# Kernel tuning notes

Hardware: AMD Instinct MI355X
Metric: run time of the kernel (lower is better)

Reference implementation:

```python
import jax, jax.numpy as jnp
import numpy as np

BN_EPS = 1e-5


def setup_inputs() -> dict:
    key = jax.random.key(0)
    k1, k2, k3, k4 = jax.random.split(key, 4)
    N, E, D_IN, D_OUT = 100000, 1600000, 128, 128
    x = jax.random.normal(k1, (N, D_IN), dtype=jnp.float32)
    edge_index = jax.random.randint(k2, (2, E), 0, N, dtype=jnp.int64)
    # GCNConv linear (glorot) + bias (zeros init in PyG)
    W = jax.random.normal(k3, (D_OUT, D_IN), dtype=jnp.float32) * (1.0 / np.sqrt(D_IN))
    b = jnp.zeros((D_OUT,), dtype=jnp.float32)
    # BatchNorm affine params
    gamma = jnp.ones((D_OUT,), dtype=jnp.float32)
    beta = jnp.zeros((D_OUT,), dtype=jnp.float32)
    return {"x": x, "edge_index": edge_index, "W": W, "b": b,
            "gamma": gamma, "beta": beta}


def reference(x, edge_index, W, b, gamma, beta):
    N = x.shape[0]
    # --- GCNConv: add self-loops, symmetric normalization ---
    loop = jnp.arange(N, dtype=edge_index.dtype)
    src = jnp.concatenate([edge_index[0], loop])  # [E+N]
    dst = jnp.concatenate([edge_index[1], loop])  # [E+N]
    deg = jax.ops.segment_sum(jnp.ones_like(dst, dtype=x.dtype), dst,
                              num_segments=N)  # in-degree incl. self-loop
    dinv = jnp.where(deg > 0, jax.lax.rsqrt(deg), 0.0)
    norm = dinv[src] * dinv[dst]  # [E+N]
    # linear transform before propagation (PyG GCNConv)
    h = x @ W.T  # [N, D_OUT]
    agg = jax.ops.segment_sum(h[src] * norm[:, None], dst, num_segments=N)
    out = agg + b
    # --- BatchNorm1d (training mode: batch statistics over nodes) ---
    mean = jnp.mean(out, axis=0)
    var = jnp.var(out, axis=0)
    out = (out - mean) * jax.lax.rsqrt(var + BN_EPS) * gamma + beta
    # --- ReLU, residual, dropout(p=0 -> identity) ---
    out = jax.nn.relu(out)
    out = out + x  # residual (in_dim == out_dim)
    return out
```

## Files before the change

kernel.cpp:

```cpp
#include <hip/hip_runtime.h>
#include <hip/hip_fp16.h>

#define BN_EPS 1e-5f

typedef unsigned int uint32;
typedef __attribute__((ext_vector_type(8))) _Float16 f16x8;
typedef __attribute__((ext_vector_type(4))) float f32x4;

union H2U { __half2 h; uint32 u; };

__device__ __forceinline__ __half2 u2h(uint32 u) { H2U c; c.u = u; return c.h; }
__device__ __forceinline__ uint32 h2u(__half2 h) { H2U c; c.h = h; return c.u; }
__device__ __forceinline__ uint32 pack2h(float a, float b) {
    return h2u(__halves2half2(__float2half_rn(a), __float2half_rn(b)));
}
__device__ __forceinline__ float h2lo(uint32 u) {
    return __half2float(__ushort_as_half((unsigned short)(u & 0xffffu)));
}
__device__ __forceinline__ float h2hi(uint32 u) {
    return __half2float(__ushort_as_half((unsigned short)(u >> 16)));
}


__global__ void __launch_bounds__(256) k_prep(const float4* __restrict__ x4, int nx4,
                                              const float4* __restrict__ w4, int nw4,
                                              const int* __restrict__ dst, int E, int NB,
                                              uint2* __restrict__ xh4, uint2* __restrict__ wh4,
                                              int* __restrict__ bcnt) {
    __shared__ int h[1024];
    int t = threadIdx.x;
    if (blockIdx.x < 256) {
        for (int i = t; i < NB; i += 256) h[i] = 0;
        __syncthreads();
        int c0 = (int)((long long)blockIdx.x * E / 256);
        int c1 = (int)((long long)(blockIdx.x + 1) * E / 256);
        for (int e = c0 + t; e < c1; e += 256) atomicAdd(&h[dst[e] >> 8], 1);
        __syncthreads();
        for (int i = t; i < NB; i += 256)
            if (h[i]) atomicAdd(&bcnt[i], h[i]);
    }
    int idx = blockIdx.x * 256 + t;
    int stride = gridDim.x * 256;
    for (int i = idx; i < nx4; i += stride) {
        float4 v = x4[i];
        xh4[i] = make_uint2(pack2h(v.x, v.y), pack2h(v.z, v.w));
    }
    for (int i = idx; i < nw4; i += stride) {
        float4 v = w4[i];
        wh4[i] = make_uint2(pack2h(v.x, v.y), pack2h(v.z, v.w));
    }
}


__global__ void k_scan1024(const int* __restrict__ in, int n, int* __restrict__ outExcl) {
    __shared__ int s[1024];
    int t = threadIdx.x;
    int v = (t < n) ? in[t] : 0;
    s[t] = v;
    __syncthreads();
    for (int off = 1; off < 1024; off <<= 1) {
        int add = (t >= off) ? s[t - off] : 0;
        __syncthreads();
        s[t] += add;
        __syncthreads();
    }
    if (t < n) outExcl[t] = s[t] - v;
    if (t == n - 1) outExcl[n] = s[t];
}


__global__ void __launch_bounds__(256) k_bscatter(const int* __restrict__ ei, int E, int NB,
                                                  const int* __restrict__ bbase,
                                                  int* __restrict__ bfill,
                                                  uint32* __restrict__ bpack) {
    __shared__ int h[1024];
    int t = threadIdx.x;
    int c0 = (int)((long long)blockIdx.x * E / gridDim.x);
    int c1 = (int)((long long)(blockIdx.x + 1) * E / gridDim.x);
    for (int i = t; i < NB; i += 256) h[i] = 0;
    __syncthreads();
    for (int e = c0 + t; e < c1; e += 256)
        atomicAdd(&h[ei[E + e] >> 8], 1);
    __syncthreads();
    for (int i = t; i < NB; i += 256) {
        int c = h[i];
        if (c > 0) h[i] = bbase[i] + atomicAdd(&bfill[i], c);
    }
    __syncthreads();
    for (int e = c0 + t; e < c1; e += 256) {
        int s = ei[e];
        int d = ei[E + e];
        int b = d >> 8;
        int pos = atomicAdd(&h[b], 1);
        bpack[pos] = ((uint32)(d & 255) << 24) | (uint32)s;
    }
}


__global__ void __launch_bounds__(256) k_csr(const uint32* __restrict__ bpack,
                                             const int* __restrict__ bbase,
                                             int N, int E,
                                             int* __restrict__ rowptr,
                                             uint32* __restrict__ dpk,
                                             int* __restrict__ col) {
    __shared__ int h[256], s[256], cur[256];
    int b = blockIdx.x;
    int t = threadIdx.x;
    int e0 = bbase[b], e1 = bbase[b + 1];
    h[t] = 0;
    __syncthreads();
    for (int e = e0 + t; e < e1; e += 256)
        atomicAdd(&h[bpack[e] >> 24], 1);
    __syncthreads();
    int cnt = h[t];
    s[t] = cnt;
    __syncthreads();
    for (int off = 1; off < 256; off <<= 1) {
        int add = (t >= off) ? s[t - off] : 0;
        __syncthreads();
        s[t] += add;
        __syncthreads();
    }
    int excl = s[t] - cnt;
    int node = (b << 8) + t;
    if (node < N) {
        rowptr[node] = e0 + excl;
        float dv = rsqrtf((float)(cnt + 1));
        dpk[node] = pack2h(dv, dv);
        if (node == N - 1) rowptr[N] = E;
    }
    cur[t] = e0 + excl;
    __syncthreads();
    for (int e = e0 + t; e < e1; e += 256) {
        uint32 p = bpack[e];
        int pos = atomicAdd(&cur[p >> 24], 1);
        col[pos] = (int)(p & 0xffffffu);
    }
}


__global__ void __launch_bounds__(256) k_agg(const uint32* __restrict__ xh,
                                             const int* __restrict__ rowptr,
                                             const int* __restrict__ col,
                                             const uint32* __restrict__ dpk,
                                             uint32* __restrict__ aggh, int N) {
    int wid = blockIdx.x * 4 + (threadIdx.x >> 6);
    if (wid >= N) return;
    int lane = threadIdx.x & 63;
    int g = lane >> 4, c = lane & 15;

    __half2 z = __float2half2_rn(0.f);
    __half2 acc0 = z, acc1 = z, acc2 = z, acc3 = z;

    int e0 = rowptr[wid], e1 = rowptr[wid + 1];
    for (int cb = e0; cb < e1; cb += 64) {
        int rem = e1 - cb;
        int lim = rem < 64 ? rem : 64;
        int sL = (lane < lim) ? col[cb + lane] : 0;
        uint32 wL = (lane < lim) ? dpk[sL] : 0;
        for (int j0 = 0; j0 < lim; j0 += 4) {
            int j = j0 + g;
            int sj = __shfl(sL, j);
            uint32 wj = (uint32)__shfl((int)wL, j);
            uint4 v = *(const uint4*)&xh[(size_t)sj * 64 + c * 4];
            acc0 = __hfma2(u2h(v.x), u2h(wj), acc0);
            acc1 = __hfma2(u2h(v.y), u2h(wj), acc1);
            acc2 = __hfma2(u2h(v.z), u2h(wj), acc2);
            acc3 = __hfma2(u2h(v.w), u2h(wj), acc3);
        }
    }
    uint32 u;
    u = __shfl_xor(h2u(acc0), 16); acc0 = __hadd2(acc0, u2h(u));
    u = __shfl_xor(h2u(acc0), 32); acc0 = __hadd2(acc0, u2h(u));
    u = __shfl_xor(h2u(acc1), 16); acc1 = __hadd2(acc1, u2h(u));
    u = __shfl_xor(h2u(acc1), 32); acc1 = __hadd2(acc1, u2h(u));
    u = __shfl_xor(h2u(acc2), 16); acc2 = __hadd2(acc2, u2h(u));
    u = __shfl_xor(h2u(acc2), 32); acc2 = __hadd2(acc2, u2h(u));
    u = __shfl_xor(h2u(acc3), 16); acc3 = __hadd2(acc3, u2h(u));
    u = __shfl_xor(h2u(acc3), 32); acc3 = __hadd2(acc3, u2h(u));

    if (g == 0) {
        float di = h2lo(dpk[wid]);
        uint4 sv = *(const uint4*)&xh[(size_t)wid * 64 + c * 4];
        uint4 o;
        o.x = pack2h(di * (di * h2lo(sv.x) + __low2float(acc0)),
                     di * (di * h2hi(sv.x) + __high2float(acc0)));
        o.y = pack2h(di * (di * h2lo(sv.y) + __low2float(acc1)),
                     di * (di * h2hi(sv.y) + __high2float(acc1)));
        o.z = pack2h(di * (di * h2lo(sv.z) + __low2float(acc2)),
                     di * (di * h2hi(sv.z) + __high2float(acc2)));
        o.w = pack2h(di * (di * h2lo(sv.w) + __low2float(acc3)),
                     di * (di * h2hi(sv.w) + __high2float(acc3)));
        *(uint4*)&aggh[(size_t)wid * 64 + c * 4] = o;
    }
}


#define STAGE_W()                                                            \
    for (int m = threadIdx.x; m < 2048; m += 256) {                          \
        int row = m >> 4, cc = m & 15;                                       \
        uint4 v = *(const uint4*)&Wh[row * 128 + cc * 8];                    \
        *(uint4*)((char*)wlds + row * 256 + ((cc * 16) ^ ((row & 7) << 4))) = v; \
    }

#define MFMA_TILE(acc, tile)                                                 \
    {                                                                        \
        int arow = (tile) * 64 + wave * 16 + lrow;                           \
        bool avalid = arow < N;                                              \
        _Pragma("unroll")                                                    \
        for (int kc = 0; kc < 4; ++kc) {                                     \
            f16x8 a;                                                         \
            if (avalid) a = *(const f16x8*)&Ah[(size_t)arow * 128 + kc * 32 + g * 8]; \
            else        a = (f16x8){0, 0, 0, 0, 0, 0, 0, 0};                 \
            _Pragma("unroll")                                                \
            for (int ct = 0; ct < 8; ++ct) {                                 \
                int row = ct * 16 + lrow;                                    \
                const f16x8 bfr = *(const f16x8*)((const char*)wlds + row * 256 \
                                   + ((kc * 64 + g * 16) ^ ((row & 7) << 4))); \
                acc[ct] = __builtin_amdgcn_mfma_f32_16x16x32_f16(a, bfr, acc[ct], 0, 0, 0); \
            }                                                                \
        }                                                                    \
    }

__global__ void __launch_bounds__(256) k_gemm_stats(const _Float16* __restrict__ Ah,
                                                    const _Float16* __restrict__ Wh,
                                                    const float* __restrict__ bias,
                                                    int N, int ntiles,
                                                    float* __restrict__ partials) {
    __shared__ uint32 wlds[8192];
    __shared__ float red[1024];
    STAGE_W();
    __syncthreads();

    int t = threadIdx.x;
    int wave = t >> 6, lane = t & 63;
    int lrow = lane & 15, g = lane >> 4;

    float bv[8];
    #pragma unroll
    for (int ct = 0; ct < 8; ++ct) bv[ct] = bias[ct * 16 + lrow];

    float s[8], sq[8];
    #pragma unroll
    for (int ct = 0; ct < 8; ++ct) { s[ct] = 0.f; sq[ct] = 0.f; }

    for (int tile = blockIdx.x; tile < ntiles; tile += gridDim.x) {
        f32x4 acc[8];
        #pragma unroll
        for (int ct = 0; ct < 8; ++ct) acc[ct] = (f32x4){0.f, 0.f, 0.f, 0.f};
        MFMA_TILE(acc, tile);
        int orow0 = tile * 64 + wave * 16 + g * 4;
        #pragma unroll
        for (int ct = 0; ct < 8; ++ct) {
            #pragma unroll
            for (int rr = 0; rr < 4; ++rr) {
                if (orow0 + rr < N) {
                    float o = acc[ct][rr] + bv[ct];
                    s[ct] += o; sq[ct] += o * o;
                }
            }
        }
    }
    #pragma unroll
    for (int ct = 0; ct < 8; ++ct) {
        s[ct] += __shfl_xor(s[ct], 16); sq[ct] += __shfl_xor(sq[ct], 16);
        s[ct] += __shfl_xor(s[ct], 32); sq[ct] += __shfl_xor(sq[ct], 32);
    }
    if (lane < 16) {
        #pragma unroll
        for (int ct = 0; ct < 8; ++ct) {
            int colI = ct * 16 + lrow;
            red[wave * 256 + colI] = s[ct];
            red[wave * 256 + 128 + colI] = sq[ct];
        }
    }
    __syncthreads();
    if (t < 256)
        partials[blockIdx.x * 256 + t] = red[t] + red[256 + t] + red[512 + t] + red[768 + t];
}


__global__ void __launch_bounds__(1024) k_bnparams(const float* __restrict__ partials, int nblk,
                                                   const float* __restrict__ gamma,
                                                   const float* __restrict__ beta,
                                                   float invN, float* __restrict__ ss) {
    __shared__ float red[1024];
    int tid = threadIdx.x;
    int colI = tid & 255, q = tid >> 8;
    int bq = nblk >> 2;
    float v0 = 0.f, v1 = 0.f, v2 = 0.f, v3 = 0.f;
    int b0 = q * bq;
    for (int b = b0; b < b0 + bq; b += 4) {
        v0 += partials[(b + 0) * 256 + colI];
        v1 += partials[(b + 1) * 256 + colI];
        v2 += partials[(b + 2) * 256 + colI];
        v3 += partials[(b + 3) * 256 + colI];
    }
    red[q * 256 + colI] = (v0 + v1) + (v2 + v3);
    __syncthreads();
    if (tid < 256) {
        float tot = red[tid] + red[256 + tid] + red[512 + tid] + red[768 + tid];
        red[tid] = tot;
    }
    __syncthreads();
    if (tid < 128) {
        float mean = red[tid] * invN;
        float var = red[128 + tid] * invN - mean * mean;
        float sc = gamma[tid] * rsqrtf(var + BN_EPS);
        ss[tid] = sc;
        ss[128 + tid] = beta[tid] - mean * sc;
    }
}

__global__ void __launch_bounds__(256) k_gemm_apply(const _Float16* __restrict__ Ah,
                                                    const _Float16* __restrict__ Wh,
                                                    const float* __restrict__ bias,
                                                    const float* __restrict__ ss,
                                                    const uint32* __restrict__ xh,
                                                    int N, int ntiles,
                                                    float* __restrict__ out) {
    __shared__ uint32 wlds[8192];
    STAGE_W();
    __syncthreads();

    int t = threadIdx.x;
    int wave = t >> 6, lane = t & 63;
    int lrow = lane & 15, g = lane >> 4;

    float bv[8], scv[8], shv[8];
    #pragma unroll
    for (int ct = 0; ct < 8; ++ct) {
        int colI = ct * 16 + lrow;
        bv[ct] = bias[colI]; scv[ct] = ss[colI]; shv[ct] = ss[128 + colI];
    }

    for (int tile = blockIdx.x; tile < ntiles; tile += gridDim.x) {
        f32x4 acc[8];
        #pragma unroll
        for (int ct = 0; ct < 8; ++ct) acc[ct] = (f32x4){0.f, 0.f, 0.f, 0.f};
        MFMA_TILE(acc, tile);
        int orow0 = tile * 64 + wave * 16 + g * 4;
        #pragma unroll
        for (int ct = 0; ct < 8; ++ct) {
            int ocol = ct * 16 + lrow;
            #pragma unroll
            for (int rr = 0; rr < 4; ++rr) {
                int r = orow0 + rr;
                if (r < N) {
                    float pre = acc[ct][rr] + bv[ct];
                    float o = fmaxf(pre * scv[ct] + shv[ct], 0.f);
                    uint32 xv = xh[(size_t)r * 64 + (ocol >> 1)];
                    float xr = (ocol & 1) ? h2hi(xv) : h2lo(xv);
                    out[(size_t)r * 128 + ocol] = o + xr;
                }
            }
        }
    }
}


extern "C" void kernel_launch(void* const* d_in, const int* in_sizes, int n_in,
                              void* d_out, int out_size, void* d_ws, size_t ws_size,
                              hipStream_t stream) {
    const float* x     = (const float*)d_in[0];
    const int*   ei    = (const int*)d_in[1];
    const float* W     = (const float*)d_in[2];
    const float* bias  = (const float*)d_in[3];
    const float* gamma = (const float*)d_in[4];
    const float* beta  = (const float*)d_in[5];
    float* out = (float*)d_out;

    const int D = 128;
    int N = in_sizes[0] / D;
    int E = in_sizes[1] / 2;
    int NB = (N + 255) >> 8;

    const int GSTATS = 256;
    const int GAPPLY = 512;

    char* ws = (char*)d_ws;
    size_t off = 0;
    auto alloc = [&](size_t bytes) -> void* {
        void* p = ws + off;
        off += (bytes + 255) & ~(size_t)255;
        return p;
    };
    uint32* xh   = (uint32*)alloc((size_t)N * 64 * sizeof(uint32));
    uint32* aggh = (uint32*)alloc((size_t)N * 64 * sizeof(uint32));
    uint32* bpack= (uint32*)alloc((size_t)E * sizeof(uint32));
    int* col     = (int*)alloc((size_t)E * sizeof(int));
    _Float16* Wh = (_Float16*)alloc((size_t)D * D * sizeof(_Float16));
    int* rowptr  = (int*)alloc((size_t)(N + 1) * sizeof(int));
    uint32* dpk  = (uint32*)alloc((size_t)N * sizeof(uint32));
    int* bbase   = (int*)alloc(1025 * sizeof(int));
    float* ss    = (float*)alloc(256 * sizeof(float));
    float* partials = (float*)alloc((size_t)GSTATS * 256 * sizeof(float));
    int* bcnt    = (int*)alloc(1024 * sizeof(int));
    int* bfill   = (int*)alloc(1024 * sizeof(int));

    hipMemsetAsync(bcnt, 0, 2 * 1024 * sizeof(int), stream);

    k_prep<<<2048, 256, 0, stream>>>((const float4*)x, N * 32, (const float4*)W, D * D / 4,
                                     ei + E, E, NB, (uint2*)xh, (uint2*)Wh, bcnt);
    k_scan1024<<<1, 1024, 0, stream>>>(bcnt, NB, bbase);
    k_bscatter<<<256, 256, 0, stream>>>(ei, E, NB, bbase, bfill, bpack);
    k_csr<<<NB, 256, 0, stream>>>(bpack, bbase, N, E, rowptr, dpk, col);
    k_agg<<<(N + 3) / 4, 256, 0, stream>>>(xh, rowptr, col, dpk, aggh, N);

    int ntiles = (N + 63) / 64;
    k_gemm_stats<<<GSTATS, 256, 0, stream>>>((const _Float16*)aggh, Wh, bias, N, ntiles, partials);
    k_bnparams<<<1, 1024, 0, stream>>>(partials, GSTATS, gamma, beta, 1.0f / (float)N, ss);
    k_gemm_apply<<<GAPPLY, 256, 0, stream>>>((const _Float16*)aggh, Wh, bias, ss, xh, N, ntiles, out);
}
```

Before: 193.1 us.

## Privatize shared histograms per wave, unroll edge gather, enlarge stats/apply grids

Shared-memory histograms and fill cursors in the prep, bucket-scatter and CSR kernels are split into one copy per wave, which cuts LDS atomic contention; per-wave offsets are derived from the per-wave counts. The aggregation loop is unrolled by four so that four independent 16-byte gathers are in flight before their FMAs. The stats and apply grid sizes are raised to 1024 blocks. The cost is four times the LDS per block, extra zeroing work, and more partials to reduce.

After: 208.1 us. +7.7%, slower.

```diff
diff --git a/kernel.cpp b/kernel.cpp
--- a/kernel.cpp
+++ b/kernel.cpp
@@ -27,17 +27,20 @@
                                               const int* __restrict__ dst, int E, int NB,
                                               uint2* __restrict__ xh4, uint2* __restrict__ wh4,
                                               int* __restrict__ bcnt) {
-    __shared__ int h[1024];
-    int t = threadIdx.x;
+    __shared__ int h[4][1024];
+    int t = threadIdx.x;
+    int wave = t >> 6;
     if (blockIdx.x < 256) {
-        for (int i = t; i < NB; i += 256) h[i] = 0;
+        for (int i = t; i < 4 * 1024; i += 256) h[i >> 10][i & 1023] = 0;
         __syncthreads();
         int c0 = (int)((long long)blockIdx.x * E / 256);
         int c1 = (int)((long long)(blockIdx.x + 1) * E / 256);
-        for (int e = c0 + t; e < c1; e += 256) atomicAdd(&h[dst[e] >> 8], 1);
-        __syncthreads();
-        for (int i = t; i < NB; i += 256)
-            if (h[i]) atomicAdd(&bcnt[i], h[i]);
+        for (int e = c0 + t; e < c1; e += 256) atomicAdd(&h[wave][dst[e] >> 8], 1);
+        __syncthreads();
+        for (int i = t; i < NB; i += 256) {
+            int s = h[0][i] + h[1][i] + h[2][i] + h[3][i];
+            if (s) atomicAdd(&bcnt[i], s);
+        }
     }
     int idx = blockIdx.x * 256 + t;
     int stride = gridDim.x * 256;
@@ -73,25 +76,33 @@
                                                   const int* __restrict__ bbase,
                                                   int* __restrict__ bfill,
                                                   uint32* __restrict__ bpack) {
-    __shared__ int h[1024];
-    int t = threadIdx.x;
+    __shared__ int h[4][1024];
+    int t = threadIdx.x;
+    int wave = t >> 6;
     int c0 = (int)((long long)blockIdx.x * E / gridDim.x);
     int c1 = (int)((long long)(blockIdx.x + 1) * E / gridDim.x);
-    for (int i = t; i < NB; i += 256) h[i] = 0;
+    for (int i = t; i < 4 * 1024; i += 256) h[i >> 10][i & 1023] = 0;
     __syncthreads();
     for (int e = c0 + t; e < c1; e += 256)
-        atomicAdd(&h[ei[E + e] >> 8], 1);
+        atomicAdd(&h[wave][ei[E + e] >> 8], 1);
     __syncthreads();
     for (int i = t; i < NB; i += 256) {
-        int c = h[i];
-        if (c > 0) h[i] = bbase[i] + atomicAdd(&bfill[i], c);
+        int n0 = h[0][i], n1 = h[1][i], n2 = h[2][i], n3 = h[3][i];
+        int tot = n0 + n1 + n2 + n3;
+        if (tot > 0) {
+            int base = bbase[i] + atomicAdd(&bfill[i], tot);
+            h[0][i] = base;
+            h[1][i] = base + n0;
+            h[2][i] = base + n0 + n1;
+            h[3][i] = base + n0 + n1 + n2;
+        }
     }
     __syncthreads();
     for (int e = c0 + t; e < c1; e += 256) {
         int s = ei[e];
         int d = ei[E + e];
         int b = d >> 8;
-        int pos = atomicAdd(&h[b], 1);
+        int pos = atomicAdd(&h[wave][b], 1);
         bpack[pos] = ((uint32)(d & 255) << 24) | (uint32)s;
     }
 }
@@ -103,16 +114,18 @@
                                              int* __restrict__ rowptr,
                                              uint32* __restrict__ dpk,
                                              int* __restrict__ col) {
-    __shared__ int h[256], s[256], cur[256];
+    __shared__ int h[4][256], s[256], cur[4][256];
     int b = blockIdx.x;
     int t = threadIdx.x;
+    int wave = t >> 6;
     int e0 = bbase[b], e1 = bbase[b + 1];
-    h[t] = 0;
+    h[0][t] = 0; h[1][t] = 0; h[2][t] = 0; h[3][t] = 0;
     __syncthreads();
     for (int e = e0 + t; e < e1; e += 256)
-        atomicAdd(&h[bpack[e] >> 24], 1);
-    __syncthreads();
-    int cnt = h[t];
+        atomicAdd(&h[wave][bpack[e] >> 24], 1);
+    __syncthreads();
+    int n0 = h[0][t], n1 = h[1][t], n2 = h[2][t], n3 = h[3][t];
+    int cnt = n0 + n1 + n2 + n3;
     s[t] = cnt;
     __syncthreads();
     for (int off = 1; off < 256; off <<= 1) {
@@ -129,15 +142,24 @@
         dpk[node] = pack2h(dv, dv);
         if (node == N - 1) rowptr[N] = E;
     }
-    cur[t] = e0 + excl;
+    cur[0][t] = e0 + excl;
+    cur[1][t] = e0 + excl + n0;
+    cur[2][t] = e0 + excl + n0 + n1;
+    cur[3][t] = e0 + excl + n0 + n1 + n2;
     __syncthreads();
     for (int e = e0 + t; e < e1; e += 256) {
         uint32 p = bpack[e];
-        int pos = atomicAdd(&cur[p >> 24], 1);
+        int pos = atomicAdd(&cur[wave][p >> 24], 1);
         col[pos] = (int)(p & 0xffffffu);
     }
 }
 
+
+#define EDGE_FMA(vv, ww)                                   \
+    acc0 = __hfma2(u2h((vv).x), u2h(ww), acc0);            \
+    acc1 = __hfma2(u2h((vv).y), u2h(ww), acc1);            \
+    acc2 = __hfma2(u2h((vv).z), u2h(ww), acc2);            \
+    acc3 = __hfma2(u2h((vv).w), u2h(ww), acc3);
 
 __global__ void __launch_bounds__(256) k_agg(const uint32* __restrict__ xh,
                                              const int* __restrict__ rowptr,
@@ -158,15 +180,25 @@
         int lim = rem < 64 ? rem : 64;
         int sL = (lane < lim) ? col[cb + lane] : 0;
         uint32 wL = (lane < lim) ? dpk[sL] : 0;
-        for (int j0 = 0; j0 < lim; j0 += 4) {
+        int j0 = 0;
+        for (; j0 + 16 <= lim; j0 += 16) {
+            int jA = j0 + g, jB = j0 + 4 + g, jC = j0 + 8 + g, jD = j0 + 12 + g;
+            int sA = __shfl(sL, jA), sB = __shfl(sL, jB);
+            int sC = __shfl(sL, jC), sD = __shfl(sL, jD);
+            uint32 wA = (uint32)__shfl((int)wL, jA), wB = (uint32)__shfl((int)wL, jB);
+            uint32 wC = (uint32)__shfl((int)wL, jC), wD = (uint32)__shfl((int)wL, jD);
+            uint4 vA = *(const uint4*)&xh[(size_t)sA * 64 + c * 4];
+            uint4 vB = *(const uint4*)&xh[(size_t)sB * 64 + c * 4];
+            uint4 vC = *(const uint4*)&xh[(size_t)sC * 64 + c * 4];
+            uint4 vD = *(const uint4*)&xh[(size_t)sD * 64 + c * 4];
+            EDGE_FMA(vA, wA); EDGE_FMA(vB, wB); EDGE_FMA(vC, wC); EDGE_FMA(vD, wD);
+        }
+        for (; j0 < lim; j0 += 4) {
             int j = j0 + g;
             int sj = __shfl(sL, j);
             uint32 wj = (uint32)__shfl((int)wL, j);
             uint4 v = *(const uint4*)&xh[(size_t)sj * 64 + c * 4];
-            acc0 = __hfma2(u2h(v.x), u2h(wj), acc0);
-            acc1 = __hfma2(u2h(v.y), u2h(wj), acc1);
-            acc2 = __hfma2(u2h(v.z), u2h(wj), acc2);
-            acc3 = __hfma2(u2h(v.w), u2h(wj), acc3);
+            EDGE_FMA(v, wj);
         }
     }
     uint32 u;
@@ -375,8 +407,8 @@
     int E = in_sizes[1] / 2;
     int NB = (N + 255) >> 8;
 
-    const int GSTATS = 256;
-    const int GAPPLY = 512;
+    const int GSTATS = 1024;
+    const int GAPPLY = 1024;
 
     char* ws = (char*)d_ws;
     size_t off = 0;
```
